# Optimization experiments

Hardware: AMD Instinct MI355X
Metric: run time of the kernel (lower is better)

The kernel has to match this reference:

```python
import jax, jax.numpy as jnp
import numpy as np

N, E, G = 100000, 1600000, 512
F_IN, H = 226, 128
BN_EPS = 1e-5

def _params(key):
    ks = jax.random.split(key, 34)
    p = {}
    dims = [(F_IN, H), (H, H), (H, H), (H, H)]
    i = 0
    for l, (din, dout) in enumerate(dims, start=1):
        p[f"W{l}a"] = jax.random.normal(ks[i], (din, dout), jnp.float32) * 0.05; i += 1
        p[f"b{l}a"] = jnp.zeros((dout,), jnp.float32)
        p[f"g{l}"] = jnp.ones((dout,), jnp.float32)
        p[f"be{l}"] = jnp.zeros((dout,), jnp.float32)
        p[f"rm{l}"] = jax.random.normal(ks[i], (dout,), jnp.float32) * 0.01; i += 1
        p[f"rv{l}"] = jnp.ones((dout,), jnp.float32)
        p[f"W{l}b"] = jax.random.normal(ks[i], (dout, dout), jnp.float32) * 0.05; i += 1
        p[f"b{l}b"] = jnp.zeros((dout,), jnp.float32)
    p["Wl"] = jax.random.normal(ks[i], (H, 1), jnp.float32) * 0.05
    p["bl"] = jnp.zeros((1,), jnp.float32)
    return p

def setup_inputs() -> dict:
    key = jax.random.key(0)
    k1, k2, k3, kp = jax.random.split(key, 4)
    inp = {
        "x": jax.random.normal(k1, (N, F_IN), jnp.float32),
        "edge_index": jax.random.randint(k2, (2, E), 0, N, jnp.int64),
        "batch": jnp.sort(jax.random.randint(k3, (N,), 0, G, jnp.int64)),
    }
    inp.update(_params(kp))
    return inp

def _gin_layer(x, src, dst, Wa, ba, g, be, rm, rv, Wb, bb):
    # GINConv (eps=0): mlp(x + sum_{j in N(i)} x_j)
    agg = jax.ops.segment_sum(x[src], dst, num_segments=N)  # [N,H] scatter-add
    h = (x + agg) @ Wa + ba
    h = g * (h - rm) * jax.lax.rsqrt(rv + BN_EPS) + be  # eval-mode BatchNorm1d
    h = jax.nn.relu(h)
    h = h @ Wb + bb
    return jax.nn.relu(h)  # outer F.relu after conv

def reference(x, edge_index, batch,
              W1a, b1a, g1, be1, rm1, rv1, W1b, b1b,
              W2a, b2a, g2, be2, rm2, rv2, W2b, b2b,
              W3a, b3a, g3, be3, rm3, rv3, W3b, b3b,
              W4a, b4a, g4, be4, rm4, rv4, W4b, b4b,
              Wl, bl):
    src, dst = edge_index[0], edge_index[1]
    h = _gin_layer(x, src, dst, W1a, b1a, g1, be1, rm1, rv1, W1b, b1b)
    h = _gin_layer(h, src, dst, W2a, b2a, g2, be2, rm2, rv2, W2b, b2b)
    h = _gin_layer(h, src, dst, W3a, b3a, g3, be3, rm3, rv3, W3b, b3b)
    h = _gin_layer(h, src, dst, W4a, b4a, g4, be4, rm4, rv4, W4b, b4b)
    # global mean pool over graphs
    sums = jax.ops.segment_sum(h, batch, num_segments=G)          # [G,H]
    cnts = jax.ops.segment_sum(jnp.ones((N,), h.dtype), batch, num_segments=G)
    pooled = sums / jnp.maximum(cnts, 1.0)[:, None]
    return pooled @ Wl + bl  # [G,1]
```

## Files before the change

kernel.cpp:

```cpp
#include <hip/hip_runtime.h>

#define NN 100000
#define NE 1600000
#define NG 512
#define FIN 226
#define HD 128
#define BN_EPS 1e-5f
#define NBUK 196
#define BCAP 10016

typedef __attribute__((ext_vector_type(8))) __bf16 bf16x8;
typedef __attribute__((ext_vector_type(8))) short short8;
typedef __attribute__((ext_vector_type(8))) unsigned short ushort8;
typedef __attribute__((ext_vector_type(4))) float f32x4;
typedef __attribute__((ext_vector_type(2))) float f32x2;

#define BC(x) __builtin_bit_cast(bf16x8, x)

__device__ inline unsigned short f2bf(float v) {
  unsigned u = __builtin_bit_cast(unsigned, v);
  return (unsigned short)((u + 0x7FFFu + ((u >> 16) & 1u)) >> 16);
}
__device__ inline float bf2f(unsigned short b) {
  return __builtin_bit_cast(float, (unsigned)b << 16);
}

__global__ __launch_bounds__(256) void k_bucket(const int* __restrict__ src,
                                                const int* __restrict__ dst,
                                                int* __restrict__ gcur,
                                                unsigned* __restrict__ pairs) {
  __shared__ int sd[4096];
  __shared__ int ss[4096];
  __shared__ int sh[NBUK];
  __shared__ int sexcl[NBUK];
  __shared__ int scur[NBUK];
  __shared__ int sbase[NBUK];
  __shared__ int wsum[4];
  const int tid = threadIdx.x;
  const int i0 = blockIdx.x * 4096;
  #pragma unroll
  for (int j = 0; j < 16; ++j) {
    int e = i0 + j * 256 + tid;
    sd[j * 256 + tid] = (e < NE) ? __builtin_nontemporal_load(dst + e) : -1;
    ss[j * 256 + tid] = (e < NE) ? __builtin_nontemporal_load(src + e) : 0;
  }
  if (tid < NBUK) sh[tid] = 0;
  __syncthreads();
  #pragma unroll
  for (int j = 0; j < 16; ++j) {
    int d = sd[j * 256 + tid];
    if (d >= 0) atomicAdd(&sh[d >> 9], 1);
  }
  __syncthreads();
  {
    int v = (tid < NBUK) ? sh[tid] : 0;
    int lane = tid & 63, w = tid >> 6;
    int incl = v;
    #pragma unroll
    for (int o = 1; o < 64; o <<= 1) {
      int u = __shfl_up(incl, o);
      if (lane >= o) incl += u;
    }
    if (lane == 63) wsum[w] = incl;
    __syncthreads();
    int off = 0;
    for (int k = 0; k < w; ++k) off += wsum[k];
    if (tid < NBUK) {
      int ex = off + incl - v;
      sexcl[tid] = ex;
      scur[tid] = ex;
      sbase[tid] = (v > 0) ? atomicAdd(&gcur[tid], v) : 0;
    }
  }
  __syncthreads();
  #pragma unroll
  for (int j = 0; j < 16; ++j) {
    int d = sd[j * 256 + tid];
    if (d >= 0) {
      int b = d >> 9;
      int lp = atomicAdd(&scur[b], 1);
      unsigned pk = ((unsigned)(d & 511) << 17) | (unsigned)ss[j * 256 + tid];
      pairs[(size_t)b * BCAP + sbase[b] + (lp - sexcl[b])] = pk;
    }
  }
}

__global__ __launch_bounds__(256) void k_pass2(const unsigned* __restrict__ pairs,
                                               const int* __restrict__ gcur,
                                               int* __restrict__ row_ptr,
                                               int* __restrict__ col_idx) {
  __shared__ unsigned spk[BCAP];
  __shared__ int h[512];
  __shared__ int cur[512];
  __shared__ int wsum[4];
  __shared__ int s_base;
  const int b = blockIdx.x;
  const int tid = threadIdx.x;
  {
    int v = (tid < NBUK) ? gcur[tid] : 0;
    int lane = tid & 63, w = tid >> 6;
    int incl = v;
    #pragma unroll
    for (int o = 1; o < 64; o <<= 1) {
      int u = __shfl_up(incl, o);
      if (lane >= o) incl += u;
    }
    if (lane == 63) wsum[w] = incl;
    __syncthreads();
    int off = 0;
    for (int k = 0; k < w; ++k) off += wsum[k];
    if (tid == b) s_base = off + incl - v;
    if (b == 0 && tid == 0) row_ptr[NN] = NE;
  }
  const int cnt = gcur[b];
  __syncthreads();
  const int base = s_base;
  for (int i = tid; i < cnt; i += 256) spk[i] = pairs[(size_t)b * BCAP + i];
  h[tid] = 0; h[tid + 256] = 0;
  __syncthreads();
  for (int i = tid; i < cnt; i += 256) atomicAdd(&h[spk[i] >> 17], 1);
  __syncthreads();
  int c0 = h[2 * tid], c1 = h[2 * tid + 1];
  {
    int v = c0 + c1;
    int lane = tid & 63, w = tid >> 6;
    int incl = v;
    #pragma unroll
    for (int o = 1; o < 64; o <<= 1) {
      int u = __shfl_up(incl, o);
      if (lane >= o) incl += u;
    }
    if (lane == 63) wsum[w] = incl;
    __syncthreads();
    int off = 0;
    for (int k = 0; k < w; ++k) off += wsum[k];
    int e0 = off + incl - v;
    int e1 = e0 + c0;
    int node0 = b * 512 + 2 * tid;
    if (node0 < NN) row_ptr[node0] = base + e0;
    if (node0 + 1 < NN) row_ptr[node0 + 1] = base + e1;
    cur[2 * tid] = e0;
    cur[2 * tid + 1] = e1;
  }
  __syncthreads();
  for (int i = tid; i < cnt; i += 256) {
    unsigned pk = spk[i];
    int dl = pk >> 17;
    int p = atomicAdd(&cur[dl], 1);
    col_idx[base + p] = (int)(pk & 0x1FFFFu);
  }
}

struct PrepArgs {
  const float* W[9];
  const float* g[9];
  const float* rv[9];
  unsigned short* out[9];
  int k0[9];
  int K[9];
  const float* ba[4];
  const float* gg[4];
  const float* be[4];
  const float* rm[4];
  const float* rvv[4];
  float* bout;
};

__global__ __launch_bounds__(256) void k_prep(PrepArgs a) {
  int id = blockIdx.x * 256 + threadIdx.x;
  if (id < 9 * 16384) {
    int chunk = id >> 14;
    int r = id & 16383;
    int kk = r >> 7;
    int n = r & 127;
    float s = a.g[chunk] ? a.g[chunk][n] * rsqrtf(a.rv[chunk][n] + BN_EPS) : 1.f;
    int kg = a.k0[chunk] + kk;
    float v = (kg < a.K[chunk]) ? a.W[chunk][(size_t)kg * HD + n] * s : 0.f;
    int idx = n * 128 + (kk ^ ((n & 7) << 3));
    a.out[chunk][idx] = f2bf(v);
  } else {
    int t = id - 9 * 16384;
    if (t < 512) {
      int l = t >> 7, c = t & 127;
      float s = a.gg[l][c] * rsqrtf(a.rvv[l][c] + BN_EPS);
      a.bout[l * 128 + c] = a.ba[l][c] * s + a.be[l][c] - a.rm[l][c] * s;
    }
  }
}

__global__ __launch_bounds__(256) void k_mgemm1(const float* __restrict__ A,
                                                const unsigned short* __restrict__ Wz,
                                                unsigned short* __restrict__ out,
                                                int K, int nchunks) {
  __shared__ unsigned short sW[16384];
  const int tid = threadIdx.x;
  const int wv = tid >> 6, ln = tid & 63;
  const int l15 = ln & 15, l4 = ln >> 4;
  const int m0 = blockIdx.x * 128 + wv * 32;
  f32x4 acc[2][8] = {};
  const int sw = (l15 & 7) << 3;
  int kofs[4];
  #pragma unroll
  for (int ks = 0; ks < 4; ++ks) kofs[ks] = (((ks * 32 + l4 * 8) ^ sw)) + l15 * 128;

  for (int c = 0; c < nchunks; ++c) {
    {
      const ushort8* src = (const ushort8*)(Wz + (size_t)c * 16384);
      ushort8* dst = (ushort8*)sW;
      #pragma unroll
      for (int i = 0; i < 8; ++i) dst[tid + i * 256] = src[tid + i * 256];
    }
    __syncthreads();
    const int kc = c * 128;
    #pragma unroll
    for (int ks = 0; ks < 4; ++ks) {
      const int kbase = kc + ks * 32 + l4 * 8;
      const bool tail = (kc + ks * 32 + 32) > K;
      short8 ah[2], al[2];
      #pragma unroll
      for (int mf = 0; mf < 2; ++mf) {
        const int row = m0 + mf * 16 + l15;
        float v[8];
        if (row < NN && !tail) {
          const f32x2* ap = (const f32x2*)(A + (size_t)row * K + kbase);
          #pragma unroll
          for (int q = 0; q < 4; ++q) {
            f32x2 t = __builtin_nontemporal_load(ap + q);
            v[2 * q] = t[0]; v[2 * q + 1] = t[1];
          }
        } else if (row < NN) {
          #pragma unroll
          for (int j = 0; j < 8; ++j) {
            int k = kbase + j;
            v[j] = (k < K) ? A[(size_t)row * K + k] : 0.f;
          }
        } else {
          #pragma unroll
          for (int j = 0; j < 8; ++j) v[j] = 0.f;
        }
        #pragma unroll
        for (int j = 0; j < 8; ++j) {
          unsigned short hb = f2bf(v[j]);
          ah[mf][j] = (short)hb;
          al[mf][j] = (short)f2bf(v[j] - bf2f(hb));
        }
      }
      #pragma unroll
      for (int n = 0; n < 8; ++n) {
        short8 bh = *(const short8*)&sW[n * 2048 + kofs[ks]];
        #pragma unroll
        for (int mf = 0; mf < 2; ++mf) {
          acc[mf][n] = __builtin_amdgcn_mfma_f32_16x16x32_bf16(BC(ah[mf]), BC(bh), acc[mf][n], 0, 0, 0);
          acc[mf][n] = __builtin_amdgcn_mfma_f32_16x16x32_bf16(BC(al[mf]), BC(bh), acc[mf][n], 0, 0, 0);
        }
      }
    }
    __syncthreads();
  }
  #pragma unroll
  for (int mf = 0; mf < 2; ++mf) {
    #pragma unroll
    for (int n = 0; n < 8; ++n) {
      const int col = n * 16 + l15;
      #pragma unroll
      for (int r = 0; r < 4; ++r) {
        const int row = m0 + mf * 16 + l4 * 4 + r;
        if (row < NN) out[(size_t)row * HD + col] = f2bf(acc[mf][n][r]);
      }
    }
  }
}

__global__ __launch_bounds__(256) void k_fused(const unsigned short* __restrict__ H,
                                               const unsigned short* __restrict__ Wzb,
                                               const float* __restrict__ bb,
                                               const unsigned short* __restrict__ Wza,
                                               unsigned short* __restrict__ Yout) {
  __shared__ __align__(16) char smem[49152];
  unsigned short* sB = (unsigned short*)smem;
  unsigned short* sA2 = (unsigned short*)(smem + 16384);
  unsigned short* sX = (unsigned short*)(smem + 32768);
  const int tid = threadIdx.x;
  const int wv = tid >> 6, ln = tid & 63;
  const int l15 = ln & 15, l4 = ln >> 4;
  const int m0 = blockIdx.x * 128 + wv * 32;
  const int sw = (l15 & 7) << 3;
  f32x4 acc2[2][8] = {};

  short8 a[2][4];
  #pragma unroll
  for (int mf = 0; mf < 2; ++mf) {
    const int row = m0 + mf * 16 + l15;
    #pragma unroll
    for (int ks = 0; ks < 4; ++ks) {
      if (row < NN) a[mf][ks] = *(const short8*)(H + (size_t)row * HD + ks * 32 + l4 * 8);
      else a[mf][ks] = short8{0, 0, 0, 0, 0, 0, 0, 0};
    }
  }

  #pragma unroll 1
  for (int p = 0; p < 2; ++p) {
    {
      ushort8* d = (ushort8*)sB;
      const ushort8* s1 = (const ushort8*)(Wzb + p * 8192);
      #pragma unroll
      for (int i = 0; i < 4; ++i) d[tid + i * 256] = s1[tid + i * 256];
    }
    {
      ushort8* d2 = (ushort8*)sA2;
      const ushort8* sa = (const ushort8*)Wza;
      #pragma unroll
      for (int i = 0; i < 4; ++i) {
        int idx = tid + i * 256;
        int n = idx >> 3, q8 = idx & 7;
        d2[idx] = sa[n * 16 + p * 8 + q8];
      }
    }
    __syncthreads();

    f32x4 acc1[2][4] = {};
    #pragma unroll
    for (int ks = 0; ks < 4; ++ks) {
      const int kof = (ks * 32 + l4 * 8) ^ sw;
      #pragma unroll
      for (int nf = 0; nf < 4; ++nf) {
        short8 bh = *(const short8*)&sB[(nf * 16 + l15) * 128 + kof];
        #pragma unroll
        for (int mf = 0; mf < 2; ++mf)
          acc1[mf][nf] = __builtin_amdgcn_mfma_f32_16x16x32_bf16(BC(a[mf][ks]), BC(bh), acc1[mf][nf], 0, 0, 0);
      }
    }
    #pragma unroll
    for (int mf = 0; mf < 2; ++mf) {
      #pragma unroll
      for (int nf = 0; nf < 4; ++nf) {
        const int colL = nf * 16 + l15;
        const float bv = bb[p * 64 + colL];
        #pragma unroll
        for (int r = 0; r < 4; ++r) {
          const int rowL = wv * 32 + mf * 16 + l4 * 4 + r;
          sX[rowL * 64 + (colL ^ ((rowL & 7) << 3))] = f2bf(fmaxf(acc1[mf][nf][r] + bv, 0.f));
        }
      }
    }
    #pragma unroll
    for (int ks2 = 0; ks2 < 2; ++ks2) {
      const int xkof = (ks2 * 32 + l4 * 8) ^ sw;
      short8 xf[2];
      #pragma unroll
      for (int mf = 0; mf < 2; ++mf) {
        const int rowL = wv * 32 + mf * 16 + l15;
        xf[mf] = *(const short8*)&sX[rowL * 64 + xkof];
      }
      #pragma unroll
      for (int nf = 0; nf < 8; ++nf) {
        short8 wh = *(const short8*)&sA2[(nf * 16 + l15) * 64 + xkof];
        #pragma unroll
        for (int mf = 0; mf < 2; ++mf)
          acc2[mf][nf] = __builtin_amdgcn_mfma_f32_16x16x32_bf16(BC(xf[mf]), BC(wh), acc2[mf][nf], 0, 0, 0);
      }
    }
    __syncthreads();
  }
  #pragma unroll
  for (int mf = 0; mf < 2; ++mf) {
    #pragma unroll
    for (int n = 0; n < 8; ++n) {
      const int col = n * 16 + l15;
      #pragma unroll
      for (int r = 0; r < 4; ++r) {
        const int row = m0 + mf * 16 + l4 * 4 + r;
        if (row < NN) Yout[(size_t)row * HD + col] = f2bf(acc2[mf][n][r]);
      }
    }
  }
}

__global__ __launch_bounds__(256) void k_agg(const unsigned short* __restrict__ y,
                                             const int* __restrict__ row_ptr,
                                             const int* __restrict__ col_idx,
                                             const float* __restrict__ bias,
                                             unsigned short* __restrict__ h) {
  const int node = blockIdx.x * 4 + (threadIdx.x >> 6);
  const int ln = threadIdx.x & 63;
  const int l15 = ln & 15, grp = ln >> 4;
  if (node >= NN) return;
  float acc[8] = {};
  const int beg = row_ptr[node], end = row_ptr[node + 1];
  int e = beg;
  for (; e + 16 <= end; e += 16) {
    const int s0 = __builtin_nontemporal_load(col_idx + e + grp);
    const int s1 = __builtin_nontemporal_load(col_idx + e + 4 + grp);
    const int s2 = __builtin_nontemporal_load(col_idx + e + 8 + grp);
    const int s3 = __builtin_nontemporal_load(col_idx + e + 12 + grp);
    const ushort8 v0 = *(const ushort8*)(y + (size_t)s0 * HD + l15 * 8);
    const ushort8 v1 = *(const ushort8*)(y + (size_t)s1 * HD + l15 * 8);
    const ushort8 v2 = *(const ushort8*)(y + (size_t)s2 * HD + l15 * 8);
    const ushort8 v3 = *(const ushort8*)(y + (size_t)s3 * HD + l15 * 8);
    #pragma unroll
    for (int j = 0; j < 8; ++j)
      acc[j] += (bf2f((unsigned short)v0[j]) + bf2f((unsigned short)v1[j])) +
                (bf2f((unsigned short)v2[j]) + bf2f((unsigned short)v3[j]));
  }
  for (; e + 8 <= end; e += 8) {
    const int s0 = __builtin_nontemporal_load(col_idx + e + grp);
    const int s1 = __builtin_nontemporal_load(col_idx + e + 4 + grp);
    const ushort8 v0 = *(const ushort8*)(y + (size_t)s0 * HD + l15 * 8);
    const ushort8 v1 = *(const ushort8*)(y + (size_t)s1 * HD + l15 * 8);
    #pragma unroll
    for (int j = 0; j < 8; ++j)
      acc[j] += bf2f((unsigned short)v0[j]) + bf2f((unsigned short)v1[j]);
  }
  if (e + 4 <= end) {
    const int s0 = __builtin_nontemporal_load(col_idx + e + grp);
    const ushort8 v0 = *(const ushort8*)(y + (size_t)s0 * HD + l15 * 8);
    #pragma unroll
    for (int j = 0; j < 8; ++j) acc[j] += bf2f((unsigned short)v0[j]);
    e += 4;
  }
  if (e + grp < end) {
    const int s0 = col_idx[e + grp];
    const ushort8 v0 = *(const ushort8*)(y + (size_t)s0 * HD + l15 * 8);
    #pragma unroll
    for (int j = 0; j < 8; ++j) acc[j] += bf2f((unsigned short)v0[j]);
  }
  #pragma unroll
  for (int j = 0; j < 8; ++j) {
    acc[j] += __shfl_xor(acc[j], 16);
    acc[j] += __shfl_xor(acc[j], 32);
  }
  const ushort8 sv = *(const ushort8*)(y + (size_t)node * HD + l15 * 8);
  const f32x4* b4 = (const f32x4*)(bias + l15 * 8);
  const f32x4 b0 = b4[0], b1 = b4[1];
  ushort8 o;
  #pragma unroll
  for (int j = 0; j < 8; ++j) {
    const float bj = (j < 4) ? b0[j] : b1[j - 4];
    o[j] = (unsigned short)f2bf(fmaxf(acc[j] + bf2f((unsigned short)sv[j]) + bj, 0.f));
  }
  if (grp == 0) *(ushort8*)(h + (size_t)node * HD + l15 * 8) = o;
}

__global__ __launch_bounds__(256) void k_bpool(const unsigned short* __restrict__ H,
                                               const unsigned short* __restrict__ Wzb,
                                               const float* __restrict__ bb,
                                               const float* __restrict__ Wl,
                                               const int* __restrict__ batch,
                                               float* __restrict__ sums,
                                               float* __restrict__ cnts) {
  __shared__ unsigned short sW[16384];
  __shared__ float sb[NG];
  __shared__ int sc[NG];
  const int tid = threadIdx.x;
  const int wv = tid >> 6, ln = tid & 63;
  const int l15 = ln & 15, l4 = ln >> 4;
  const int m0 = blockIdx.x * 128 + wv * 32;
  const int sw = (l15 & 7) << 3;
  for (int i = tid; i < NG; i += 256) { sb[i] = 0.f; sc[i] = 0; }
  {
    const ushort8* src = (const ushort8*)Wzb;
    ushort8* dst = (ushort8*)sW;
    #pragma unroll
    for (int i = 0; i < 8; ++i) dst[tid + i * 256] = src[tid + i * 256];
  }
  __syncthreads();
  f32x4 acc[2][8] = {};
  #pragma unroll
  for (int ks = 0; ks < 4; ++ks) {
    const int kbase = ks * 32 + l4 * 8;
    short8 a[2];
    #pragma unroll
    for (int mf = 0; mf < 2; ++mf) {
      const int row = m0 + mf * 16 + l15;
      if (row < NN) a[mf] = *(const short8*)(H + (size_t)row * HD + kbase);
      else a[mf] = short8{0, 0, 0, 0, 0, 0, 0, 0};
    }
    const int kof = (kbase ^ sw) + l15 * 128;
    #pragma unroll
    for (int n = 0; n < 8; ++n) {
      short8 bh = *(const short8*)&sW[n * 2048 + kof];
      #pragma unroll
      for (int mf = 0; mf < 2; ++mf)
        acc[mf][n] = __builtin_amdgcn_mfma_f32_16x16x32_bf16(BC(a[mf]), BC(bh), acc[mf][n], 0, 0, 0);
    }
  }
  float pdot[2][4] = {};
  #pragma unroll
  for (int mf = 0; mf < 2; ++mf) {
    #pragma unroll
    for (int n = 0; n < 8; ++n) {
      const int col = n * 16 + l15;
      const float bv = bb[col];
      const float wl = Wl[col];
      #pragma unroll
      for (int r = 0; r < 4; ++r)
        pdot[mf][r] += fmaxf(acc[mf][n][r] + bv, 0.f) * wl;
    }
  }
  #pragma unroll
  for (int mf = 0; mf < 2; ++mf) {
    #pragma unroll
    for (int r = 0; r < 4; ++r) {
      float d = pdot[mf][r];
      d += __shfl_xor(d, 1);
      d += __shfl_xor(d, 2);
      d += __shfl_xor(d, 4);
      d += __shfl_xor(d, 8);
      if (l15 == 0) {
        const int row = m0 + mf * 16 + l4 * 4 + r;
        if (row < NN) {
          const int g = batch[row];
          atomicAdd(&sb[g], d);
          atomicAdd(&sc[g], 1);
        }
      }
    }
  }
  __syncthreads();
  for (int i = tid; i < NG; i += 256)
    if (sc[i]) { atomicAdd(&sums[i], sb[i]); atomicAdd(&cnts[i], (float)sc[i]); }
}

__global__ void k_final(const float* __restrict__ sums, const float* __restrict__ cnts,
                        const float* __restrict__ bl, float* __restrict__ out) {
  int g = blockIdx.x * 256 + threadIdx.x;
  if (g < NG) out[g] = sums[g] / fmaxf(cnts[g], 1.f) + bl[0];
}

extern "C" void kernel_launch(void* const* d_in, const int* in_sizes, int n_in,
                              void* d_out, int out_size, void* d_ws, size_t ws_size,
                              hipStream_t stream) {
  const float* x = (const float*)d_in[0];
  const int* edges = (const int*)d_in[1];
  const int* batch = (const int*)d_in[2];
  const int* e_src = edges;
  const int* e_dst = edges + NE;
  const float* Wl = (const float*)d_in[35];
  const float* bl = (const float*)d_in[36];
  float* out = (float*)d_out;
  auto P = [&](int l, int which) -> const float* {
    return (const float*)d_in[3 + (l - 1) * 8 + which];
  };

  char* ws = (char*)d_ws;
  size_t off = 0;
  auto take = [&](size_t bytes) -> void* {
    void* p = ws + off;
    off = (off + bytes + 255) & ~(size_t)255;
    return p;
  };
  unsigned short* Y = (unsigned short*)take((size_t)NN * HD * 2);
  unsigned short* H = (unsigned short*)take((size_t)NN * HD * 2);
  int* row_ptr = (int*)take((size_t)(NN + 1) * 4);
  int* col_idx = (int*)take((size_t)NE * 4);
  unsigned* pairs = (unsigned*)take((size_t)NBUK * BCAP * 4);
  int* gcur = (int*)take((size_t)NBUK * 4);
  unsigned short* Wza[4];
  unsigned short* Wzb[4];
  Wza[0] = (unsigned short*)take((size_t)2 * 16384 * 2);
  for (int l = 1; l < 4; ++l) Wza[l] = (unsigned short*)take((size_t)16384 * 2);
  for (int l = 0; l < 4; ++l) Wzb[l] = (unsigned short*)take((size_t)16384 * 2);
  float* bf = (float*)take((size_t)4 * HD * 4);
  float* psum = (float*)take((size_t)NG * 4 * 2);
  float* pcnt = psum + NG;

  hipMemsetAsync(gcur, 0, (size_t)NBUK * 4, stream);
  k_bucket<<<(NE + 4095) / 4096, 256, 0, stream>>>(e_src, e_dst, gcur, pairs);
  k_pass2<<<NBUK, 256, 0, stream>>>(pairs, gcur, row_ptr, col_idx);

  PrepArgs pa;
  for (int c = 0; c < 9; ++c) {
    if (c < 2) { pa.W[c] = P(1, 0); pa.g[c] = P(1, 2); pa.rv[c] = P(1, 5);
                 pa.out[c] = Wza[0] + c * 16384; pa.k0[c] = c * 128; pa.K[c] = FIN; }
    else if (c < 5) { int l = c - 1; pa.W[c] = P(l + 1, 0); pa.g[c] = P(l + 1, 2);
                      pa.rv[c] = P(l + 1, 5); pa.out[c] = Wza[l]; pa.k0[c] = 0; pa.K[c] = HD; }
    else { int l = c - 5; pa.W[c] = P(l + 1, 6); pa.g[c] = nullptr; pa.rv[c] = nullptr;
           pa.out[c] = Wzb[l]; pa.k0[c] = 0; pa.K[c] = HD; }
  }
  for (int l = 0; l < 4; ++l) {
    pa.ba[l] = P(l + 1, 1); pa.gg[l] = P(l + 1, 2); pa.be[l] = P(l + 1, 3);
    pa.rm[l] = P(l + 1, 4); pa.rvv[l] = P(l + 1, 5);
  }
  pa.bout = bf;
  k_prep<<<(9 * 16384 + 512 + 255) / 256, 256, 0, stream>>>(pa);

  hipMemsetAsync(psum, 0, (size_t)NG * 8, stream);

  const int grid = (NN + 127) / 128;
  k_mgemm1<<<grid, 256, 0, stream>>>(x, Wza[0], Y, FIN, 2);
  for (int l = 1; l <= 3; ++l) {
    k_agg<<<NN / 4, 256, 0, stream>>>(Y, row_ptr, col_idx, bf + (l - 1) * HD, H);
    k_fused<<<grid, 256, 0, stream>>>(H, Wzb[l - 1], P(l, 7), Wza[l], Y);
  }
  k_agg<<<NN / 4, 256, 0, stream>>>(Y, row_ptr, col_idx, bf + 3 * HD, H);
  k_bpool<<<grid, 256, 0, stream>>>(H, Wzb[3], P(4, 7), Wl, batch, psum, pcnt);
  k_final<<<(NG + 255) / 256, 256, 0, stream>>>(psum, pcnt, bl, out);
}
```

Measured before the change: 470.3 us.

## Merge edge bucketing with first-layer GEMM and fold memsets into prep kernel

```diff
diff --git a/kernel.cpp b/kernel.cpp
--- a/kernel.cpp
+++ b/kernel.cpp
@@ -8,6 +8,8 @@
 #define BN_EPS 1e-5f
 #define NBUK 196
 #define BCAP 10016
+#define BKB 391
+#define G1B 782
 
 typedef __attribute__((ext_vector_type(8))) __bf16 bf16x8;
 typedef __attribute__((ext_vector_type(8))) short short8;
@@ -23,132 +25,6 @@
 }
 __device__ inline float bf2f(unsigned short b) {
   return __builtin_bit_cast(float, (unsigned)b << 16);
-}
-
-__global__ __launch_bounds__(256) void k_bucket(const int* __restrict__ src,
-                                                const int* __restrict__ dst,
-                                                int* __restrict__ gcur,
-                                                unsigned* __restrict__ pairs) {
-  __shared__ int sd[4096];
-  __shared__ int ss[4096];
-  __shared__ int sh[NBUK];
-  __shared__ int sexcl[NBUK];
-  __shared__ int scur[NBUK];
-  __shared__ int sbase[NBUK];
-  __shared__ int wsum[4];
-  const int tid = threadIdx.x;
-  const int i0 = blockIdx.x * 4096;
-  #pragma unroll
-  for (int j = 0; j < 16; ++j) {
-    int e = i0 + j * 256 + tid;
-    sd[j * 256 + tid] = (e < NE) ? __builtin_nontemporal_load(dst + e) : -1;
-    ss[j * 256 + tid] = (e < NE) ? __builtin_nontemporal_load(src + e) : 0;
-  }
-  if (tid < NBUK) sh[tid] = 0;
-  __syncthreads();
-  #pragma unroll
-  for (int j = 0; j < 16; ++j) {
-    int d = sd[j * 256 + tid];
-    if (d >= 0) atomicAdd(&sh[d >> 9], 1);
-  }
-  __syncthreads();
-  {
-    int v = (tid < NBUK) ? sh[tid] : 0;
-    int lane = tid & 63, w = tid >> 6;
-    int incl = v;
-    #pragma unroll
-    for (int o = 1; o < 64; o <<= 1) {
-      int u = __shfl_up(incl, o);
-      if (lane >= o) incl += u;
-    }
-    if (lane == 63) wsum[w] = incl;
-    __syncthreads();
-    int off = 0;
-    for (int k = 0; k < w; ++k) off += wsum[k];
-    if (tid < NBUK) {
-      int ex = off + incl - v;
-      sexcl[tid] = ex;
-      scur[tid] = ex;
-      sbase[tid] = (v > 0) ? atomicAdd(&gcur[tid], v) : 0;
-    }
-  }
-  __syncthreads();
-  #pragma unroll
-  for (int j = 0; j < 16; ++j) {
-    int d = sd[j * 256 + tid];
-    if (d >= 0) {
-      int b = d >> 9;
-      int lp = atomicAdd(&scur[b], 1);
-      unsigned pk = ((unsigned)(d & 511) << 17) | (unsigned)ss[j * 256 + tid];
-      pairs[(size_t)b * BCAP + sbase[b] + (lp - sexcl[b])] = pk;
-    }
-  }
-}
-
-__global__ __launch_bounds__(256) void k_pass2(const unsigned* __restrict__ pairs,
-                                               const int* __restrict__ gcur,
-                                               int* __restrict__ row_ptr,
-                                               int* __restrict__ col_idx) {
-  __shared__ unsigned spk[BCAP];
-  __shared__ int h[512];
-  __shared__ int cur[512];
-  __shared__ int wsum[4];
-  __shared__ int s_base;
-  const int b = blockIdx.x;
-  const int tid = threadIdx.x;
-  {
-    int v = (tid < NBUK) ? gcur[tid] : 0;
-    int lane = tid & 63, w = tid >> 6;
-    int incl = v;
-    #pragma unroll
-    for (int o = 1; o < 64; o <<= 1) {
-      int u = __shfl_up(incl, o);
-      if (lane >= o) incl += u;
-    }
-    if (lane == 63) wsum[w] = incl;
-    __syncthreads();
-    int off = 0;
-    for (int k = 0; k < w; ++k) off += wsum[k];
-    if (tid == b) s_base = off + incl - v;
-    if (b == 0 && tid == 0) row_ptr[NN] = NE;
-  }
-  const int cnt = gcur[b];
-  __syncthreads();
-  const int base = s_base;
-  for (int i = tid; i < cnt; i += 256) spk[i] = pairs[(size_t)b * BCAP + i];
-  h[tid] = 0; h[tid + 256] = 0;
-  __syncthreads();
-  for (int i = tid; i < cnt; i += 256) atomicAdd(&h[spk[i] >> 17], 1);
-  __syncthreads();
-  int c0 = h[2 * tid], c1 = h[2 * tid + 1];
-  {
-    int v = c0 + c1;
-    int lane = tid & 63, w = tid >> 6;
-    int incl = v;
-    #pragma unroll
-    for (int o = 1; o < 64; o <<= 1) {
-      int u = __shfl_up(incl, o);
-      if (lane >= o) incl += u;
-    }
-    if (lane == 63) wsum[w] = incl;
-    __syncthreads();
-    int off = 0;
-    for (int k = 0; k < w; ++k) off += wsum[k];
-    int e0 = off + incl - v;
-    int e1 = e0 + c0;
-    int node0 = b * 512 + 2 * tid;
-    if (node0 < NN) row_ptr[node0] = base + e0;
-    if (node0 + 1 < NN) row_ptr[node0 + 1] = base + e1;
-    cur[2 * tid] = e0;
-    cur[2 * tid + 1] = e1;
-  }
-  __syncthreads();
-  for (int i = tid; i < cnt; i += 256) {
-    unsigned pk = spk[i];
-    int dl = pk >> 17;
-    int p = atomicAdd(&cur[dl], 1);
-    col_idx[base + p] = (int)(pk & 0x1FFFFu);
-  }
 }
 
 struct PrepArgs {
@@ -166,7 +42,8 @@
   float* bout;
 };
 
-__global__ __launch_bounds__(256) void k_prep(PrepArgs a) {
+__global__ __launch_bounds__(256) void k_prep(PrepArgs a, int* __restrict__ gcur,
+                                              float* __restrict__ psum) {
   int id = blockIdx.x * 256 + threadIdx.x;
   if (id < 9 * 16384) {
     int chunk = id >> 14;
@@ -184,91 +61,288 @@
       int l = t >> 7, c = t & 127;
       float s = a.gg[l][c] * rsqrtf(a.rvv[l][c] + BN_EPS);
       a.bout[l * 128 + c] = a.ba[l][c] * s + a.be[l][c] - a.rm[l][c] * s;
-    }
-  }
-}
-
-__global__ __launch_bounds__(256) void k_mgemm1(const float* __restrict__ A,
-                                                const unsigned short* __restrict__ Wz,
-                                                unsigned short* __restrict__ out,
-                                                int K, int nchunks) {
-  __shared__ unsigned short sW[16384];
+    } else if (t < 512 + 2 * NG) {
+      psum[t - 512] = 0.f;
+    } else if (t < 512 + 2 * NG + NBUK) {
+      gcur[t - 512 - 2 * NG] = 0;
+    }
+  }
+}
+
+__global__ __launch_bounds__(256) void k_b1(const int* __restrict__ src,
+                                            const int* __restrict__ dst,
+                                            int* __restrict__ gcur,
+                                            unsigned* __restrict__ pairs,
+                                            const float* __restrict__ A,
+                                            const unsigned short* __restrict__ Wz,
+                                            unsigned short* __restrict__ out) {
+  __shared__ __align__(16) char smem[36096];
   const int tid = threadIdx.x;
-  const int wv = tid >> 6, ln = tid & 63;
-  const int l15 = ln & 15, l4 = ln >> 4;
-  const int m0 = blockIdx.x * 128 + wv * 32;
-  f32x4 acc[2][8] = {};
-  const int sw = (l15 & 7) << 3;
-  int kofs[4];
-  #pragma unroll
-  for (int ks = 0; ks < 4; ++ks) kofs[ks] = (((ks * 32 + l4 * 8) ^ sw)) + l15 * 128;
-
-  for (int c = 0; c < nchunks; ++c) {
+  if (blockIdx.x < BKB) {
+    int* sd = (int*)smem;
+    int* ss = (int*)(smem + 16384);
+    int* sh = (int*)(smem + 32768);
+    int* sexcl = sh + NBUK;
+    int* scur = sexcl + NBUK;
+    int* sbase = scur + NBUK;
+    int* wsum = sbase + NBUK;
+    const int i0 = blockIdx.x * 4096;
+    #pragma unroll
+    for (int j = 0; j < 16; ++j) {
+      int e = i0 + j * 256 + tid;
+      sd[j * 256 + tid] = (e < NE) ? __builtin_nontemporal_load(dst + e) : -1;
+      ss[j * 256 + tid] = (e < NE) ? __builtin_nontemporal_load(src + e) : 0;
+    }
+    if (tid < NBUK) sh[tid] = 0;
+    __syncthreads();
+    #pragma unroll
+    for (int j = 0; j < 16; ++j) {
+      int d = sd[j * 256 + tid];
+      if (d >= 0) atomicAdd(&sh[d >> 9], 1);
+    }
+    __syncthreads();
     {
-      const ushort8* src = (const ushort8*)(Wz + (size_t)c * 16384);
-      ushort8* dst = (ushort8*)sW;
-      #pragma unroll
-      for (int i = 0; i < 8; ++i) dst[tid + i * 256] = src[tid + i * 256];
+      int v = (tid < NBUK) ? sh[tid] : 0;
+      int lane = tid & 63, w = tid >> 6;
+      int incl = v;
+      #pragma unroll
+      for (int o = 1; o < 64; o <<= 1) {
+        int u = __shfl_up(incl, o);
+        if (lane >= o) incl += u;
+      }
+      if (lane == 63) wsum[w] = incl;
+      __syncthreads();
+      int off = 0;
+      for (int k = 0; k < w; ++k) off += wsum[k];
+      if (tid < NBUK) {
+        int ex = off + incl - v;
+        sexcl[tid] = ex;
+        scur[tid] = ex;
+        sbase[tid] = (v > 0) ? atomicAdd(&gcur[tid], v) : 0;
+      }
     }
     __syncthreads();
-    const int kc = c * 128;
-    #pragma unroll
-    for (int ks = 0; ks < 4; ++ks) {
-      const int kbase = kc + ks * 32 + l4 * 8;
-      const bool tail = (kc + ks * 32 + 32) > K;
-      short8 ah[2], al[2];
-      #pragma unroll
-      for (int mf = 0; mf < 2; ++mf) {
-        const int row = m0 + mf * 16 + l15;
-        float v[8];
-        if (row < NN && !tail) {
-          const f32x2* ap = (const f32x2*)(A + (size_t)row * K + kbase);
-          #pragma unroll
-          for (int q = 0; q < 4; ++q) {
-            f32x2 t = __builtin_nontemporal_load(ap + q);
-            v[2 * q] = t[0]; v[2 * q + 1] = t[1];
+    #pragma unroll
+    for (int j = 0; j < 16; ++j) {
+      int d = sd[j * 256 + tid];
+      if (d >= 0) {
+        int b = d >> 9;
+        int lp = atomicAdd(&scur[b], 1);
+        unsigned pk = ((unsigned)(d & 511) << 17) | (unsigned)ss[j * 256 + tid];
+        pairs[(size_t)b * BCAP + sbase[b] + (lp - sexcl[b])] = pk;
+      }
+    }
+  } else {
+    unsigned short* sW = (unsigned short*)smem;
+    const int wv = tid >> 6, ln = tid & 63;
+    const int l15 = ln & 15, l4 = ln >> 4;
+    const int m0 = (blockIdx.x - BKB) * 128 + wv * 32;
+    f32x4 acc[2][8] = {};
+    const int sw = (l15 & 7) << 3;
+    int kofs[4];
+    #pragma unroll
+    for (int ks = 0; ks < 4; ++ks) kofs[ks] = (((ks * 32 + l4 * 8) ^ sw)) + l15 * 128;
+
+    for (int c = 0; c < 2; ++c) {
+      {
+        const ushort8* srcw = (const ushort8*)(Wz + (size_t)c * 16384);
+        ushort8* dstw = (ushort8*)sW;
+        #pragma unroll
+        for (int i = 0; i < 8; ++i) dstw[tid + i * 256] = srcw[tid + i * 256];
+      }
+      __syncthreads();
+      const int kc = c * 128;
+      #pragma unroll
+      for (int ks = 0; ks < 4; ++ks) {
+        const int kbase = kc + ks * 32 + l4 * 8;
+        const bool tail = (kc + ks * 32 + 32) > FIN;
+        short8 ah[2], al[2];
+        #pragma unroll
+        for (int mf = 0; mf < 2; ++mf) {
+          const int row = m0 + mf * 16 + l15;
+          float v[8];
+          if (row < NN && !tail) {
+            const f32x2* ap = (const f32x2*)(A + (size_t)row * FIN + kbase);
+            #pragma unroll
+            for (int q = 0; q < 4; ++q) {
+              f32x2 t = __builtin_nontemporal_load(ap + q);
+              v[2 * q] = t[0]; v[2 * q + 1] = t[1];
+            }
+          } else if (row < NN) {
+            #pragma unroll
+            for (int j = 0; j < 8; ++j) {
+              int k = kbase + j;
+              v[j] = (k < FIN) ? A[(size_t)row * FIN + k] : 0.f;
+            }
+          } else {
+            #pragma unroll
+            for (int j = 0; j < 8; ++j) v[j] = 0.f;
           }
-        } else if (row < NN) {
           #pragma unroll
           for (int j = 0; j < 8; ++j) {
-            int k = kbase + j;
-            v[j] = (k < K) ? A[(size_t)row * K + k] : 0.f;
+            unsigned short hb = f2bf(v[j]);
+            ah[mf][j] = (short)hb;
+            al[mf][j] = (short)f2bf(v[j] - bf2f(hb));
           }
-        } else {
-          #pragma unroll
-          for (int j = 0; j < 8; ++j) v[j] = 0.f;
         }
         #pragma unroll
-        for (int j = 0; j < 8; ++j) {
-          unsigned short hb = f2bf(v[j]);
-          ah[mf][j] = (short)hb;
-          al[mf][j] = (short)f2bf(v[j] - bf2f(hb));
+        for (int n = 0; n < 8; ++n) {
+          short8 bh = *(const short8*)&sW[n * 2048 + kofs[ks]];
+          #pragma unroll
+          for (int mf = 0; mf < 2; ++mf) {
+            acc[mf][n] = __builtin_amdgcn_mfma_f32_16x16x32_bf16(BC(ah[mf]), BC(bh), acc[mf][n], 0, 0, 0);
+            acc[mf][n] = __builtin_amdgcn_mfma_f32_16x16x32_bf16(BC(al[mf]), BC(bh), acc[mf][n], 0, 0, 0);
+          }
         }
       }
+      __syncthreads();
+    }
+    #pragma unroll
+    for (int mf = 0; mf < 2; ++mf) {
       #pragma unroll
       for (int n = 0; n < 8; ++n) {
-        short8 bh = *(const short8*)&sW[n * 2048 + kofs[ks]];
+        const int col = n * 16 + l15;
         #pragma unroll
-        for (int mf = 0; mf < 2; ++mf) {
-          acc[mf][n] = __builtin_amdgcn_mfma_f32_16x16x32_bf16(BC(ah[mf]), BC(bh), acc[mf][n], 0, 0, 0);
-          acc[mf][n] = __builtin_amdgcn_mfma_f32_16x16x32_bf16(BC(al[mf]), BC(bh), acc[mf][n], 0, 0, 0);
+        for (int r = 0; r < 4; ++r) {
+          const int row = m0 + mf * 16 + l4 * 4 + r;
+          if (row < NN) out[(size_t)row * HD + col] = f2bf(acc[mf][n][r]);
         }
       }
     }
+  }
+}
+
+__global__ __launch_bounds__(256) void k_pass2(const unsigned* __restrict__ pairs,
+                                               const int* __restrict__ gcur,
+                                               int* __restrict__ row_ptr,
+                                               int* __restrict__ col_idx) {
+  __shared__ unsigned spk[BCAP];
+  __shared__ int h[512];
+  __shared__ int cur[512];
+  __shared__ int wsum[4];
+  __shared__ int s_base;
+  const int b = blockIdx.x;
+  const int tid = threadIdx.x;
+  {
+    int v = (tid < NBUK) ? gcur[tid] : 0;
+    int lane = tid & 63, w = tid >> 6;
+    int incl = v;
+    #pragma unroll
+    for (int o = 1; o < 64; o <<= 1) {
+      int u = __shfl_up(incl, o);
+      if (lane >= o) incl += u;
+    }
+    if (lane == 63) wsum[w] = incl;
     __syncthreads();
+    int off = 0;
+    for (int k = 0; k < w; ++k) off += wsum[k];
+    if (tid == b) s_base = off + incl - v;
+    if (b == 0 && tid == 0) row_ptr[NN] = NE;
+  }
+  const int cnt = gcur[b];
+  __syncthreads();
+  const int base = s_base;
+  for (int i = tid; i < cnt; i += 256) spk[i] = pairs[(size_t)b * BCAP + i];
+  h[tid] = 0; h[tid + 256] = 0;
+  __syncthreads();
+  for (int i = tid; i < cnt; i += 256) atomicAdd(&h[spk[i] >> 17], 1);
+  __syncthreads();
+  int c0 = h[2 * tid], c1 = h[2 * tid + 1];
+  {
+    int v = c0 + c1;
+    int lane = tid & 63, w = tid >> 6;
+    int incl = v;
+    #pragma unroll
+    for (int o = 1; o < 64; o <<= 1) {
+      int u = __shfl_up(incl, o);
+      if (lane >= o) incl += u;
+    }
+    if (lane == 63) wsum[w] = incl;
+    __syncthreads();
+    int off = 0;
+    for (int k = 0; k < w; ++k) off += wsum[k];
+    int e0 = off + incl - v;
+    int e1 = e0 + c0;
+    int node0 = b * 512 + 2 * tid;
+    if (node0 < NN) row_ptr[node0] = base + e0;
+    if (node0 + 1 < NN) row_ptr[node0 + 1] = base + e1;
+    cur[2 * tid] = e0;
+    cur[2 * tid + 1] = e1;
+  }
+  __syncthreads();
+  for (int i = tid; i < cnt; i += 256) {
+    unsigned pk = spk[i];
+    int dl = pk >> 17;
+    int p = atomicAdd(&cur[dl], 1);
+    col_idx[base + p] = (int)((pk & 0x1FFFFu) << 8);
+  }
+}
+
+__global__ __launch_bounds__(256) void k_agg(const unsigned short* __restrict__ y,
+                                             const int* __restrict__ row_ptr,
+                                             const int* __restrict__ col_idx,
+                                             const float* __restrict__ bias,
+                                             unsigned short* __restrict__ h) {
+  const int node = blockIdx.x * 4 + (threadIdx.x >> 6);
+  const int ln = threadIdx.x & 63;
+  const int l15 = ln & 15, grp = ln >> 4;
+  if (node >= NN) return;
+  const char* yb = (const char*)y;
+  const int lo = l15 * 16;
+  float acc[8] = {};
+  const int beg = row_ptr[node], end = row_ptr[node + 1];
+  int e = beg;
+  for (; e + 16 <= end; e += 16) {
+    const int s0 = __builtin_nontemporal_load(col_idx + e + grp);
+    const int s1 = __builtin_nontemporal_load(col_idx + e + 4 + grp);
+    const int s2 = __builtin_nontemporal_load(col_idx + e + 8 + grp);
+    const int s3 = __builtin_nontemporal_load(col_idx + e + 12 + grp);
+    const ushort8 v0 = *(const ushort8*)(yb + s0 + lo);
+    const ushort8 v1 = *(const ushort8*)(yb + s1 + lo);
+    const ushort8 v2 = *(const ushort8*)(yb + s2 + lo);
+    const ushort8 v3 = *(const ushort8*)(yb + s3 + lo);
+    #pragma unroll
+    for (int j = 0; j < 8; ++j)
+      acc[j] += (bf2f((unsigned short)v0[j]) + bf2f((unsigned short)v1[j])) +
+                (bf2f((unsigned short)v2[j]) + bf2f((unsigned short)v3[j]));
+  }
+  for (; e + 8 <= end; e += 8) {
+    const int s0 = __builtin_nontemporal_load(col_idx + e + grp);
+    const int s1 = __builtin_nontemporal_load(col_idx + e + 4 + grp);
+    const ushort8 v0 = *(const ushort8*)(yb + s0 + lo);
+    const ushort8 v1 = *(const ushort8*)(yb + s1 + lo);
+    #pragma unroll
+    for (int j = 0; j < 8; ++j)
+      acc[j] += bf2f((unsigned short)v0[j]) + bf2f((unsigned short)v1[j]);
+  }
+  if (e + 4 <= end) {
+    const int s0 = __builtin_nontemporal_load(col_idx + e + grp);
+    const ushort8 v0 = *(const ushort8*)(yb + s0 + lo);
+    #pragma unroll
+    for (int j = 0; j < 8; ++j) acc[j] += bf2f((unsigned short)v0[j]);
+    e += 4;
+  }
+  if (e + grp < end) {
+    const int s0 = col_idx[e + grp];
+    const ushort8 v0 = *(const ushort8*)(yb + s0 + lo);
+    #pragma unroll
+    for (int j = 0; j < 8; ++j) acc[j] += bf2f((unsigned short)v0[j]);
   }
   #pragma unroll
-  for (int mf = 0; mf < 2; ++mf) {
-    #pragma unroll
-    for (int n = 0; n < 8; ++n) {
-      const int col = n * 16 + l15;
-      #pragma unroll
-      for (int r = 0; r < 4; ++r) {
-        const int row = m0 + mf * 16 + l4 * 4 + r;
-        if (row < NN) out[(size_t)row * HD + col] = f2bf(acc[mf][n][r]);
-      }
-    }
-  }
+  for (int j = 0; j < 8; ++j) {
+    acc[j] += __shfl_xor(acc[j], 16);
+    acc[j] += __shfl_xor(acc[j], 32);
+  }
+  const ushort8 sv = *(const ushort8*)(y + (size_t)node * HD + l15 * 8);
+  const f32x4* b4 = (const f32x4*)(bias + l15 * 8);
+  const f32x4 b0 = b4[0], b1 = b4[1];
+  ushort8 o;
+  #pragma unroll
+  for (int j = 0; j < 8; ++j) {
+    const float bj = (j < 4) ? b0[j] : b1[j - 4];
+    o[j] = (unsigned short)f2bf(fmaxf(acc[j] + bf2f((unsigned short)sv[j]) + bj, 0.f));
+  }
+  if (grp == 0) *(ushort8*)(h + (size_t)node * HD + l15 * 8) = o;
 }
 
 __global__ __launch_bounds__(256) void k_fused(const unsigned short* __restrict__ H,
@@ -374,71 +448,6 @@
       }
     }
   }
-}
-
-__global__ __launch_bounds__(256) void k_agg(const unsigned short* __restrict__ y,
-                                             const int* __restrict__ row_ptr,
-                                             const int* __restrict__ col_idx,
-                                             const float* __restrict__ bias,
-                                             unsigned short* __restrict__ h) {
-  const int node = blockIdx.x * 4 + (threadIdx.x >> 6);
-  const int ln = threadIdx.x & 63;
-  const int l15 = ln & 15, grp = ln >> 4;
-  if (node >= NN) return;
-  float acc[8] = {};
-  const int beg = row_ptr[node], end = row_ptr[node + 1];
-  int e = beg;
-  for (; e + 16 <= end; e += 16) {
-    const int s0 = __builtin_nontemporal_load(col_idx + e + grp);
-    const int s1 = __builtin_nontemporal_load(col_idx + e + 4 + grp);
-    const int s2 = __builtin_nontemporal_load(col_idx + e + 8 + grp);
-    const int s3 = __builtin_nontemporal_load(col_idx + e + 12 + grp);
-    const ushort8 v0 = *(const ushort8*)(y + (size_t)s0 * HD + l15 * 8);
-    const ushort8 v1 = *(const ushort8*)(y + (size_t)s1 * HD + l15 * 8);
-    const ushort8 v2 = *(const ushort8*)(y + (size_t)s2 * HD + l15 * 8);
-    const ushort8 v3 = *(const ushort8*)(y + (size_t)s3 * HD + l15 * 8);
-    #pragma unroll
-    for (int j = 0; j < 8; ++j)
-      acc[j] += (bf2f((unsigned short)v0[j]) + bf2f((unsigned short)v1[j])) +
-                (bf2f((unsigned short)v2[j]) + bf2f((unsigned short)v3[j]));
-  }
-  for (; e + 8 <= end; e += 8) {
-    const int s0 = __builtin_nontemporal_load(col_idx + e + grp);
-    const int s1 = __builtin_nontemporal_load(col_idx + e + 4 + grp);
-    const ushort8 v0 = *(const ushort8*)(y + (size_t)s0 * HD + l15 * 8);
-    const ushort8 v1 = *(const ushort8*)(y + (size_t)s1 * HD + l15 * 8);
-    #pragma unroll
-    for (int j = 0; j < 8; ++j)
-      acc[j] += bf2f((unsigned short)v0[j]) + bf2f((unsigned short)v1[j]);
-  }
-  if (e + 4 <= end) {
-    const int s0 = __builtin_nontemporal_load(col_idx + e + grp);
-    const ushort8 v0 = *(const ushort8*)(y + (size_t)s0 * HD + l15 * 8);
-    #pragma unroll
-    for (int j = 0; j < 8; ++j) acc[j] += bf2f((unsigned short)v0[j]);
-    e += 4;
-  }
-  if (e + grp < end) {
-    const int s0 = col_idx[e + grp];
-    const ushort8 v0 = *(const ushort8*)(y + (size_t)s0 * HD + l15 * 8);
-    #pragma unroll
-    for (int j = 0; j < 8; ++j) acc[j] += bf2f((unsigned short)v0[j]);
-  }
-  #pragma unroll
-  for (int j = 0; j < 8; ++j) {
-    acc[j] += __shfl_xor(acc[j], 16);
-    acc[j] += __shfl_xor(acc[j], 32);
-  }
-  const ushort8 sv = *(const ushort8*)(y + (size_t)node * HD + l15 * 8);
-  const f32x4* b4 = (const f32x4*)(bias + l15 * 8);
-  const f32x4 b0 = b4[0], b1 = b4[1];
-  ushort8 o;
-  #pragma unroll
-  for (int j = 0; j < 8; ++j) {
-    const float bj = (j < 4) ? b0[j] : b1[j - 4];
-    o[j] = (unsigned short)f2bf(fmaxf(acc[j] + bf2f((unsigned short)sv[j]) + bj, 0.f));
-  }
-  if (grp == 0) *(ushort8*)(h + (size_t)node * HD + l15 * 8) = o;
 }
 
 __global__ __launch_bounds__(256) void k_bpool(const unsigned short* __restrict__ H,
@@ -564,10 +573,6 @@
   float* psum = (float*)take((size_t)NG * 4 * 2);
   float* pcnt = psum + NG;
 
-  hipMemsetAsync(gcur, 0, (size_t)NBUK * 4, stream);
-  k_bucket<<<(NE + 4095) / 4096, 256, 0, stream>>>(e_src, e_dst, gcur, pairs);
-  k_pass2<<<NBUK, 256, 0, stream>>>(pairs, gcur, row_ptr, col_idx);
-
   PrepArgs pa;
   for (int c = 0; c < 9; ++c) {
     if (c < 2) { pa.W[c] = P(1, 0); pa.g[c] = P(1, 2); pa.rv[c] = P(1, 5);
@@ -582,12 +587,12 @@
     pa.rm[l] = P(l + 1, 4); pa.rvv[l] = P(l + 1, 5);
   }
   pa.bout = bf;
-  k_prep<<<(9 * 16384 + 512 + 255) / 256, 256, 0, stream>>>(pa);
-
-  hipMemsetAsync(psum, 0, (size_t)NG * 8, stream);
+  k_prep<<<(9 * 16384 + 512 + 2 * NG + NBUK + 255) / 256, 256, 0, stream>>>(pa, gcur, psum);
+
+  k_b1<<<BKB + G1B, 256, 0, stream>>>(e_src, e_dst, gcur, pairs, x, Wza[0], Y);
+  k_pass2<<<NBUK, 256, 0, stream>>>(pairs, gcur, row_ptr, col_idx);
 
   const int grid = (NN + 127) / 128;
-  k_mgemm1<<<grid, 256, 0, stream>>>(x, Wza[0], Y, FIN, 2);
   for (int l = 1; l <= 3; ++l) {
     k_agg<<<NN / 4, 256, 0, stream>>>(Y, row_ptr, col_idx, bf + (l - 1) * HD, H);
     k_fused<<<grid, 256, 0, stream>>>(H, Wzb[l - 1], P(l, 7), Wza[l], Y);
```

Result: faster. 443.6 us (median of 2 runs) (-5.7%).
